# Kernel tuning notes

Measured on AMD Instinct MI355X. Metric: run time of the kernel, lower is better.

## Reference

```python
import jax, jax.numpy as jnp
import numpy as np
import math

ITER = 5
ALPHA = 2.0
C = 128
B, H, W = 64, 40, 96


def _conv(x, w, pad_h, pad_w):
    # x: [B,C,H,W], w: [O,I,kh,kw]
    return jax.lax.conv_general_dilated(
        x, w, window_strides=(1, 1),
        padding=[(pad_h, pad_h), (pad_w, pad_w)],
        dimension_numbers=("NCHW", "OIHW", "NCHW"))


def setup_inputs() -> dict:
    key = jax.random.key(0)
    k = jax.random.split(key, 5)
    bound = math.sqrt(2.0 / (C * 9 * 5))
    x = jax.random.normal(k[0], (B, C, H, W), dtype=jnp.float32)
    wd = jax.random.uniform(k[1], (ITER, C, C, 1, 9), jnp.float32, -bound, bound)
    wu = jax.random.uniform(k[2], (ITER, C, C, 1, 9), jnp.float32, -bound, bound)
    wr = jax.random.uniform(k[3], (ITER, C, C, 9, 1), jnp.float32, -bound, bound)
    wl = jax.random.uniform(k[4], (ITER, C, C, 9, 1), jnp.float32, -bound, bound)
    return {"x": x, "wd": wd, "wu": wu, "wr": wr, "wl": wl}


def reference(x, wd, wu, wr, wl):
    h, w = x.shape[-2], x.shape[-1]
    y = x
    # downward: circular shift of rows by +offset == roll(-offset) along H
    for i in range(ITER):
        off = h // 2 ** (ITER - i)
        y = y + ALPHA * jax.nn.relu(_conv(jnp.roll(y, -off, axis=2), wd[i], 0, 4))
    # upward: rows shifted by -offset == roll(+offset)
    for i in range(ITER):
        off = h // 2 ** (ITER - i)
        y = y + ALPHA * jax.nn.relu(_conv(jnp.roll(y, off, axis=2), wu[i], 0, 4))
    # rightward: cols shifted by +offset == roll(-offset) along W
    for i in range(ITER):
        off = w // 2 ** (ITER - i)
        y = y + ALPHA * jax.nn.relu(_conv(jnp.roll(y, -off, axis=3), wr[i], 4, 0))
    # leftward: cols shifted by -offset == roll(+offset)
    for i in range(ITER):
        off = w // 2 ** (ITER - i)
        y = y + ALPHA * jax.nn.relu(_conv(jnp.roll(y, off, axis=3), wl[i], 4, 0))
    return y
```

## Files before the change

### kernel.cpp

```cpp
#include <hip/hip_runtime.h>
#include <cstdint>
#include <cstddef>

#define CH 128
#define HH 40
#define WW 96
#define BB 64
#define HW (HH*WW)
#define CHW ((size_t)CH*HW)

typedef _Float16 half8  __attribute__((ext_vector_type(8)));
typedef _Float16 half4v __attribute__((ext_vector_type(4)));
typedef float    float4v __attribute__((ext_vector_type(4)));

#define MFMA16(a,b,c) __builtin_amdgcn_mfma_f32_16x16x32_f16((a),(b),(c),0,0,0)

#define SPLIT_SCALE 2048.0f
#define INV_SPLIT   (1.0f/2048.0f)

#define NHWC_HALVES (BB*HH*WW*CH)
#define WSTEP_F     (CH*CH*9)
#define WFRAG_HALVES (20*9*4*8*64*8)


__global__ __launch_bounds__(256) void prep_weights(
    const float* __restrict__ wd, const float* __restrict__ wu,
    const float* __restrict__ wr, const float* __restrict__ wl,
    _Float16* __restrict__ WH, _Float16* __restrict__ WM)
{
    const int bx = blockIdx.x;
    const int s = bx / 9, t = bx % 9;
    const float* src;
    if (s < 5)       src = wd + (size_t)s*WSTEP_F;
    else if (s < 10) src = wu + (size_t)(s-5)*WSTEP_F;
    else if (s < 15) src = wr + (size_t)(s-10)*WSTEP_F;
    else             src = wl + (size_t)(s-15)*WSTEP_F;

    for (int idx = threadIdx.x; idx < 2048; idx += 256) {
        const int lane = idx & 63;
        const int mt   = (idx >> 6) & 7;
        const int kq   = idx >> 9;
        const int co   = mt*16 + (lane & 15);
        const int cib  = kq*32 + (lane >> 4)*8;
        const int F    = ((((s*9 + t)*4 + kq)*8 + mt)*64 + lane)*8;
        #pragma unroll
        for (int j = 0; j < 8; ++j) {
            const float w = src[(size_t)(co*CH + (cib + j))*9 + t];
            const _Float16 h = (_Float16)w;
            WH[F + j] = h;
            WM[F + j] = (_Float16)((w - (float)h) * SPLIT_SCALE);
        }
    }
}

__global__ __launch_bounds__(256) void prep_acts(
    const float* __restrict__ x, _Float16* __restrict__ H, _Float16* __restrict__ M)
{
    __shared__ float tile[CH][33];
    const int wt = blockIdx.x, h = blockIdx.y, b = blockIdx.z;
    const int tid = threadIdx.x;
    {
        const int wl = tid & 31, c0 = tid >> 5;
        for (int it = 0; it < 16; ++it) {
            const int ci = it*8 + c0;
            tile[ci][wl] = x[((size_t)(b*CH + ci)*HH + h)*WW + wt*32 + wl];
        }
    }
    __syncthreads();
    {
        const int ci = tid & 127, w0 = tid >> 7;
        for (int it = 0; it < 16; ++it) {
            const int wl = it*2 + w0;
            const float v = tile[ci][wl];
            const _Float16 hh = (_Float16)v;
            const int o = ((b*HH + h)*WW + wt*32 + wl)*CH + ci;
            H[o] = hh;
            M[o] = (_Float16)((v - (float)hh) * SPLIT_SCALE);
        }
    }
}

__global__ __launch_bounds__(256, 2) void hconv_mfma(
    const _Float16* __restrict__ srcH, const _Float16* __restrict__ srcM,
    _Float16* __restrict__ dstH, _Float16* __restrict__ dstM,
    const _Float16* __restrict__ WH, const _Float16* __restrict__ WM,
    int s, int hoff)
{
    __shared__ _Float16 sB[2][104*136];
    const int h = blockIdx.x, b = blockIdx.y;
    const int tid = threadIdx.x;
    const int hp = (h + hoff) % HH;

    {
        const int l = tid & 15, r0 = tid >> 4;
        for (int it = 0; it < 7; ++it) {
            const int r = it*16 + r0;
            if (r < 104) {
                half8 vh = {}, vm = {};
                if (r >= 4 && r < 100) {
                    const int off = ((b*HH + hp)*WW + (r-4))*CH + l*8;
                    vh = *(const half8*)(srcH + off);
                    vm = *(const half8*)(srcM + off);
                }
                *(half8*)&sB[0][r*136 + l*8] = vh;
                *(half8*)&sB[1][r*136 + l*8] = vm;
            }
        }
    }
    __syncthreads();

    const int lane = tid & 63, wave = tid >> 6;
    const int n = lane & 15, quad = lane >> 4;
    const int mgrp = wave & 1, ngrp = wave >> 1;
    const int qb = quad*8;

    float4v acc0[4][3], acc1[4][3];
    #pragma unroll
    for (int i = 0; i < 4; ++i)
        #pragma unroll
        for (int j = 0; j < 3; ++j) {
            acc0[i][j] = (float4v){0.f,0.f,0.f,0.f};
            acc1[i][j] = (float4v){0.f,0.f,0.f,0.f};
        }

    int rowb[3], rb136[3];
    #pragma unroll
    for (int j = 0; j < 3; ++j) {
        rowb[j]  = (ngrp*3 + j)*16 + n;
        rb136[j] = rowb[j]*136;
    }

    const size_t Fb = (size_t)s*147456 + (size_t)(mgrp*2048 + lane*8);

    half8 Wh[2][4], Wm[2][4];
    #pragma unroll
    for (int i = 0; i < 4; ++i) {
        Wh[0][i] = *(const half8*)(WH + Fb + i*512);
        Wm[0][i] = *(const half8*)(WM + Fb + i*512);
    }
    half8 pbh = *(const half8*)&sB[0][rb136[0] + qb];
    half8 pbm = *(const half8*)&sB[1][rb136[0] + qb];

    for (int t = 0; t < 9; ++t) {
        #pragma unroll
        for (int kq = 0; kq < 4; ++kq) {
            const int it  = t*4 + kq;
            const int itn = (it < 35) ? it + 1 : 35;
            const int pc  = kq & 1;
            const int pn  = pc ^ 1;
            {
                const _Float16* nH = WH + Fb + (size_t)itn*4096;
                const _Float16* nM = WM + Fb + (size_t)itn*4096;
                #pragma unroll
                for (int i = 0; i < 4; ++i) {
                    Wh[pn][i] = *(const half8*)(nH + i*512);
                    Wm[pn][i] = *(const half8*)(nM + i*512);
                }
            }
            const int tn = itn >> 2, kqn = itn & 3;
            #pragma unroll
            for (int j = 0; j < 3; ++j) {
                const half8 bh = pbh, bm = pbm;
                int nro;
                if (j < 2) nro = rb136[j+1] + t*136 + kq*32 + qb;
                else       nro = rb136[0]   + tn*136 + kqn*32 + qb;
                pbh = *(const half8*)&sB[0][nro];
                pbm = *(const half8*)&sB[1][nro];
                __builtin_amdgcn_s_setprio(1);
                #pragma unroll
                for (int i = 0; i < 4; ++i) {
                    acc0[i][j] = MFMA16(Wh[pc][i], bh, acc0[i][j]);
                    acc1[i][j] = MFMA16(Wh[pc][i], bm, acc1[i][j]);
                    acc1[i][j] = MFMA16(Wm[pc][i], bh, acc1[i][j]);
                }
                __builtin_amdgcn_s_setprio(0);
            }
        }
    }

    const int spbase = (b*HH + h)*WW;
    #pragma unroll
    for (int i = 0; i < 4; ++i) {
        const int co = (mgrp*4 + i)*16 + quad*4;
        #pragma unroll
        for (int j = 0; j < 3; ++j) {
            const int w  = (ngrp*3 + j)*16 + n;
            const int sp = (spbase + w)*CH + co;
            const half4v oh = *(const half4v*)(srcH + sp);
            const half4v om = *(const half4v*)(srcM + sp);
            half4v zh, zm;
            #pragma unroll
            for (int r = 0; r < 4; ++r) {
                const float v = acc0[i][j][r] + acc1[i][j][r]*INV_SPLIT;
                const float y = (float)oh[r] + (float)om[r]*INV_SPLIT;
                const float z = y + 2.0f*fmaxf(v, 0.0f);
                const _Float16 a = (_Float16)z;
                zh[r] = a;
                zm[r] = (_Float16)((z - (float)a)*SPLIT_SCALE);
            }
            *(half4v*)(dstH + sp) = zh;
            *(half4v*)(dstM + sp) = zm;
        }
    }
}

__global__ __launch_bounds__(256, 2) void vconv_mfma(
    const _Float16* __restrict__ srcH, const _Float16* __restrict__ srcM,
    _Float16* __restrict__ dstH, _Float16* __restrict__ dstM,
    const _Float16* __restrict__ WH, const _Float16* __restrict__ WM,
    int s, int woff, int final, float* __restrict__ f32out)
{
    __shared__ _Float16 sB[2][2*56*136];
    const int wp = blockIdx.x, b = blockIdx.y;
    const int tid = threadIdx.x;

    {
        const int l = tid & 15, r0 = tid >> 4;
        for (int it = 0; it < 7; ++it) {
            const int r = it*16 + r0;
            const int col = r / 56, p = r % 56;
            half8 vh = {}, vm = {};
            if (p >= 4 && p < 44) {
                const int wsrc = (wp*2 + col + woff) % WW;
                const int off = ((b*HH + (p-4))*WW + wsrc)*CH + l*8;
                vh = *(const half8*)(srcH + off);
                vm = *(const half8*)(srcM + off);
            }
            *(half8*)&sB[0][(col*56 + p)*136 + l*8] = vh;
            *(half8*)&sB[1][(col*56 + p)*136 + l*8] = vm;
        }
    }
    __syncthreads();

    const int lane = tid & 63, wave = tid >> 6;
    const int n = lane & 15, quad = lane >> 4;
    const int mgrp = wave & 1, col = wave >> 1;
    const int qb = quad*8;

    float4v acc0[4][3], acc1[4][3];
    #pragma unroll
    for (int i = 0; i < 4; ++i)
        #pragma unroll
        for (int j = 0; j < 3; ++j) {
            acc0[i][j] = (float4v){0.f,0.f,0.f,0.f};
            acc1[i][j] = (float4v){0.f,0.f,0.f,0.f};
        }

    int rowb[3], rb136[3];
    #pragma unroll
    for (int j = 0; j < 3; ++j) {
        rowb[j]  = col*56 + j*16 + n;
        rb136[j] = rowb[j]*136;
    }

    const size_t Fb = (size_t)s*147456 + (size_t)(mgrp*2048 + lane*8);

    half8 Wh[2][4], Wm[2][4];
    #pragma unroll
    for (int i = 0; i < 4; ++i) {
        Wh[0][i] = *(const half8*)(WH + Fb + i*512);
        Wm[0][i] = *(const half8*)(WM + Fb + i*512);
    }
    half8 pbh = *(const half8*)&sB[0][rb136[0] + qb];
    half8 pbm = *(const half8*)&sB[1][rb136[0] + qb];

    for (int t = 0; t < 9; ++t) {
        #pragma unroll
        for (int kq = 0; kq < 4; ++kq) {
            const int it  = t*4 + kq;
            const int itn = (it < 35) ? it + 1 : 35;
            const int pc  = kq & 1;
            const int pn  = pc ^ 1;
            {
                const _Float16* nH = WH + Fb + (size_t)itn*4096;
                const _Float16* nM = WM + Fb + (size_t)itn*4096;
                #pragma unroll
                for (int i = 0; i < 4; ++i) {
                    Wh[pn][i] = *(const half8*)(nH + i*512);
                    Wm[pn][i] = *(const half8*)(nM + i*512);
                }
            }
            const int tn = itn >> 2, kqn = itn & 3;
            #pragma unroll
            for (int j = 0; j < 3; ++j) {
                const half8 bh = pbh, bm = pbm;
                int nro;
                if (j < 2) nro = rb136[j+1] + t*136 + kq*32 + qb;
                else       nro = rb136[0]   + tn*136 + kqn*32 + qb;
                pbh = *(const half8*)&sB[0][nro];
                pbm = *(const half8*)&sB[1][nro];
                __builtin_amdgcn_s_setprio(1);
                #pragma unroll
                for (int i = 0; i < 4; ++i) {
                    acc0[i][j] = MFMA16(Wh[pc][i], bh, acc0[i][j]);
                    acc1[i][j] = MFMA16(Wh[pc][i], bm, acc1[i][j]);
                    acc1[i][j] = MFMA16(Wm[pc][i], bh, acc1[i][j]);
                }
                __builtin_amdgcn_s_setprio(0);
            }
        }
    }

    const int w_out = wp*2 + col;
    #pragma unroll
    for (int i = 0; i < 4; ++i) {
        const int co = (mgrp*4 + i)*16 + quad*4;
        #pragma unroll
        for (int j = 0; j < 3; ++j) {
            const int h_out = j*16 + n;
            if (h_out < HH) {
                const int sp = ((b*HH + h_out)*WW + w_out)*CH + co;
                const half4v oh = *(const half4v*)(srcH + sp);
                const half4v om = *(const half4v*)(srcM + sp);
                if (final) {
                    float4v z4;
                    #pragma unroll
                    for (int r = 0; r < 4; ++r) {
                        const float v = acc0[i][j][r] + acc1[i][j][r]*INV_SPLIT;
                        const float y = (float)oh[r] + (float)om[r]*INV_SPLIT;
                        z4[r] = y + 2.0f*fmaxf(v, 0.0f);
                    }
                    *(float4v*)(f32out + sp) = z4;
                } else {
                    half4v zh, zm;
                    #pragma unroll
                    for (int r = 0; r < 4; ++r) {
                        const float v = acc0[i][j][r] + acc1[i][j][r]*INV_SPLIT;
                        const float y = (float)oh[r] + (float)om[r]*INV_SPLIT;
                        const float z = y + 2.0f*fmaxf(v, 0.0f);
                        const _Float16 a = (_Float16)z;
                        zh[r] = a;
                        zm[r] = (_Float16)((z - (float)a)*SPLIT_SCALE);
                    }
                    *(half4v*)(dstH + sp) = zh;
                    *(half4v*)(dstM + sp) = zm;
                }
            }
        }
    }
}

__global__ __launch_bounds__(256) void nhwc_to_nchw(
    const float* __restrict__ src, float* __restrict__ dst)
{
    __shared__ float tile[32][133];
    const int wt = blockIdx.x, h = blockIdx.y, b = blockIdx.z;
    const int tid = threadIdx.x;
    {
        const int ci = tid & 127, w0 = tid >> 7;
        for (int it = 0; it < 16; ++it) {
            const int wl = it*2 + w0;
            tile[wl][ci] = src[((size_t)(b*HH + h)*WW + wt*32 + wl)*CH + ci];
        }
    }
    __syncthreads();
    {
        const int wl = tid & 31, c0 = tid >> 5;
        for (int it = 0; it < 16; ++it) {
            const int ci = it*8 + c0;
            dst[((size_t)(b*CH + ci)*HH + h)*WW + wt*32 + wl] = tile[wl][ci];
        }
    }
}

__global__ __launch_bounds__(256) void hconv_step(
    const float* __restrict__ src, const float* __restrict__ wgt,
    float* __restrict__ dst, int hoff)
{
    __shared__ float ld[CH][104];
    const int h = blockIdx.x, b = blockIdx.y, tid = threadIdx.x;
    const int hp = (h + hoff) % HH;
    const float* srow = src + (size_t)b*CHW + (size_t)hp*WW;
    for (int idx = tid; idx < CH*24; idx += 256) {
        int ci = idx / 24, j = idx % 24;
        float4 v = *reinterpret_cast<const float4*>(srow + (size_t)ci*HW + j*4);
        *reinterpret_cast<float4*>(&ld[ci][4 + 4*j]) = v;
    }
    if (tid < CH) {
        *reinterpret_cast<float4*>(&ld[tid][0])   = make_float4(0.f,0.f,0.f,0.f);
        *reinterpret_cast<float4*>(&ld[tid][100]) = make_float4(0.f,0.f,0.f,0.f);
    }
    __syncthreads();
    const int tx = tid & 7, ty = tid >> 3;
    const int w0 = tx*12, co0 = ty*4;
    float acc[4][12];
    #pragma unroll
    for (int c = 0; c < 4; ++c)
        #pragma unroll
        for (int k = 0; k < 12; ++k) acc[c][k] = 0.f;
    const float* wb = wgt + (size_t)co0*(CH*9);
    for (int ci = 0; ci < CH; ++ci) {
        float xr[20];
        #pragma unroll
        for (int j = 0; j < 5; ++j) {
            float4 v = *reinterpret_cast<const float4*>(&ld[ci][w0 + 4*j]);
            xr[4*j+0]=v.x; xr[4*j+1]=v.y; xr[4*j+2]=v.z; xr[4*j+3]=v.w;
        }
        #pragma unroll
        for (int c = 0; c < 4; ++c) {
            const float* wp = wb + (size_t)c*(CH*9) + ci*9;
            #pragma unroll
            for (int t = 0; t < 9; ++t) {
                const float wv = wp[t];
                #pragma unroll
                for (int k = 0; k < 12; ++k) acc[c][k] = fmaf(wv, xr[k+t], acc[c][k]);
            }
        }
    }
    const size_t obase = (size_t)b*CHW + (size_t)h*WW + w0;
    #pragma unroll
    for (int c = 0; c < 4; ++c) {
        const size_t o = obase + (size_t)(co0 + c)*HW;
        #pragma unroll
        for (int j = 0; j < 3; ++j) {
            float4 s = *reinterpret_cast<const float4*>(src + o + 4*j);
            float4 r;
            r.x = s.x + 2.f*fmaxf(acc[c][4*j+0], 0.f);
            r.y = s.y + 2.f*fmaxf(acc[c][4*j+1], 0.f);
            r.z = s.z + 2.f*fmaxf(acc[c][4*j+2], 0.f);
            r.w = s.w + 2.f*fmaxf(acc[c][4*j+3], 0.f);
            *reinterpret_cast<float4*>(dst + o + 4*j) = r;
        }
    }
}

__global__ __launch_bounds__(256) void vconv_step(
    const float* __restrict__ src, const float* __restrict__ wgt,
    float* __restrict__ dst, int woff)
{
    __shared__ float ld[CH][2][48];
    const int w0 = blockIdx.x*2, b = blockIdx.y, tid = threadIdx.x;
    const int w1 = (w0 + woff) % WW, w2 = (w0 + 1 + woff) % WW;
    const float* sb = src + (size_t)b*CHW;
    for (int idx = tid; idx < CH*HH; idx += 256) {
        int ci = idx / HH, hh = idx % HH;
        const float* p = sb + (size_t)ci*HW + (size_t)hh*WW;
        ld[ci][0][4 + hh] = p[w1];
        ld[ci][1][4 + hh] = p[w2];
    }
    if (tid < CH) {
        #pragma unroll
        for (int j = 0; j < 4; ++j) {
            ld[tid][0][j]=0.f; ld[tid][0][44+j]=0.f;
            ld[tid][1][j]=0.f; ld[tid][1][44+j]=0.f;
        }
    }
    __syncthreads();
    const int tx = tid & 7, ty = tid >> 3;
    const int wi = tx >> 2, h0 = (tx & 3)*10, co0 = ty*4;
    float acc[4][10];
    #pragma unroll
    for (int c = 0; c < 4; ++c)
        #pragma unroll
        for (int k = 0; k < 10; ++k) acc[c][k] = 0.f;
    const float* wb = wgt + (size_t)co0*(CH*9);
    for (int ci = 0; ci < CH; ++ci) {
        float xr[18];
        #pragma unroll
        for (int j = 0; j < 18; ++j) xr[j] = ld[ci][wi][h0 + j];
        #pragma unroll
        for (int c = 0; c < 4; ++c) {
            const float* wp = wb + (size_t)c*(CH*9) + ci*9;
            #pragma unroll
            for (int t = 0; t < 9; ++t) {
                const float wv = wp[t];
                #pragma unroll
                for (int k = 0; k < 10; ++k) acc[c][k] = fmaf(wv, xr[k+t], acc[c][k]);
            }
        }
    }
    #pragma unroll
    for (int c = 0; c < 4; ++c) {
        const size_t o = (size_t)b*CHW + (size_t)(co0 + c)*HW + (size_t)h0*WW + (w0 + wi);
        #pragma unroll
        for (int k = 0; k < 10; ++k) {
            const float s = src[o + (size_t)k*WW];
            dst[o + (size_t)k*WW] = s + 2.f*fmaxf(acc[c][k], 0.f);
        }
    }
}

extern "C" void kernel_launch(void* const* d_in, const int* in_sizes, int n_in,
                              void* d_out, int out_size, void* d_ws, size_t ws_size,
                              hipStream_t stream)
{
    const float* x  = (const float*)d_in[0];
    const float* wd = (const float*)d_in[1];
    const float* wu = (const float*)d_in[2];
    const float* wr = (const float*)d_in[3];
    const float* wl = (const float*)d_in[4];

    const size_t NEED = 125829120ULL + 2ULL*WFRAG_HALVES*2ULL;

    if (ws_size >= NEED) {
        _Float16* HA  = (_Float16*)d_ws;
        _Float16* MA  = HA + NHWC_HALVES;
        _Float16* WHp = (_Float16*)((char*)d_ws + 125829120ULL);
        _Float16* WMp = WHp + WFRAG_HALVES;
        _Float16* HB  = (_Float16*)d_out;
        _Float16* MB  = HB + NHWC_HALVES;
        float* f32tmp = (float*)d_ws;

        prep_weights<<<dim3(180), 256, 0, stream>>>(wd, wu, wr, wl, WHp, WMp);
        prep_acts<<<dim3(3, HH, BB), 256, 0, stream>>>(x, HA, MA);

        const int hoffs[10] = {1,2,5,10,20, 39,38,35,30,20};
        for (int s = 0; s < 10; ++s) {
            const _Float16* sH = (s & 1) ? HB : HA;
            const _Float16* sM = (s & 1) ? MB : MA;
            _Float16* dH = (s & 1) ? HA : HB;
            _Float16* dM = (s & 1) ? MA : MB;
            hconv_mfma<<<dim3(HH, BB), 256, 0, stream>>>(sH, sM, dH, dM,
                                                         WHp, WMp, s, hoffs[s]);
        }
        const int woffs[10] = {3,6,12,24,48, 93,90,84,72,48};
        for (int k = 0; k < 10; ++k) {
            const int s = 10 + k;
            const _Float16* sH = (s & 1) ? HB : HA;
            const _Float16* sM = (s & 1) ? MB : MA;
            _Float16* dH = (s & 1) ? HA : HB;
            _Float16* dM = (s & 1) ? MA : MB;
            const int fin = (s == 19);
            vconv_mfma<<<dim3(WW/2, BB), 256, 0, stream>>>(sH, sM, dH, dM,
                                                           WHp, WMp, s, woffs[k],
                                                           fin, f32tmp);
        }
        nhwc_to_nchw<<<dim3(3, HH, BB), 256, 0, stream>>>(f32tmp, (float*)d_out);
    } else {
        float* out = (float*)d_out;
        float* ws  = (float*)d_ws;
        const size_t WSTEP = (size_t)WSTEP_F;
        const int hoffs[5] = {1, 2, 5, 10, 20};
        const int woffs[5] = {3, 6, 12, 24, 48};
        dim3 hgrid(HH, BB), vgrid(WW/2, BB);
        const float* src = x;
        int step = 0;
        for (int i = 0; i < 5; ++i) {
            float* dst = (step & 1) ? out : ws;
            hconv_step<<<hgrid, 256, 0, stream>>>(src, wd + i*WSTEP, dst, hoffs[i]);
            src = dst; ++step;
        }
        for (int i = 0; i < 5; ++i) {
            float* dst = (step & 1) ? out : ws;
            hconv_step<<<hgrid, 256, 0, stream>>>(src, wu + i*WSTEP, dst, (HH - hoffs[i]) % HH);
            src = dst; ++step;
        }
        for (int i = 0; i < 5; ++i) {
            float* dst = (step & 1) ? out : ws;
            vconv_step<<<vgrid, 256, 0, stream>>>(src, wr + i*WSTEP, dst, woffs[i]);
            src = dst; ++step;
        }
        for (int i = 0; i < 5; ++i) {
            float* dst = (step & 1) ? out : ws;
            vconv_step<<<vgrid, 256, 0, stream>>>(src, wl + i*WSTEP, dst, (WW - woffs[i]) % WW);
            src = dst; ++step;
        }
    }
}
```

Before: 4.576 ms.

## Use direct global-to-LDS loads with XOR swizzle and pack vconv output rows

Both conv kernels now stage their input tiles with global_load_lds, which writes 16-byte chunks straight into shared memory without passing through registers. The old 136-half row padding is replaced by an XOR swizzle of the column chunk, and the halo rows are zeroed separately. In vconv the two columns' 40 rows are packed together so 80 outputs split into 5 16-row tiles instead of 6 padded ones, with one wave group doing only two tiles. This cuts staging instructions, LDS footprint and wasted MFMA work, at the cost of uneven load across waves and more complex addressing.

```diff
diff --git a/kernel.cpp b/kernel.cpp
--- a/kernel.cpp
+++ b/kernel.cpp
@@ -21,6 +21,13 @@
 #define NHWC_HALVES (BB*HH*WW*CH)
 #define WSTEP_F     (CH*CH*9)
 #define WFRAG_HALVES (20*9*4*8*64*8)
+
+__device__ __forceinline__ void gload16(const _Float16* g, _Float16* l) {
+    __builtin_amdgcn_global_load_lds(
+        (const __attribute__((address_space(1))) void*)g,
+        (__attribute__((address_space(3))) void*)l,
+        16, 0, 0);
+}
 
 
 __global__ __launch_bounds__(256) void prep_weights(
@@ -86,33 +93,34 @@
     const _Float16* __restrict__ WH, const _Float16* __restrict__ WM,
     int s, int hoff)
 {
-    __shared__ _Float16 sB[2][104*136];
+    __shared__ _Float16 sB[2][104*128];
     const int h = blockIdx.x, b = blockIdx.y;
     const int tid = threadIdx.x;
     const int hp = (h + hoff) % HH;
+    const int lane = tid & 63, wave = tid >> 6;
 
     {
-        const int l = tid & 15, r0 = tid >> 4;
-        for (int it = 0; it < 7; ++it) {
-            const int r = it*16 + r0;
-            if (r < 104) {
-                half8 vh = {}, vm = {};
-                if (r >= 4 && r < 100) {
-                    const int off = ((b*HH + hp)*WW + (r-4))*CH + l*8;
-                    vh = *(const half8*)(srcH + off);
-                    vm = *(const half8*)(srcM + off);
-                }
-                *(half8*)&sB[0][r*136 + l*8] = vh;
-                *(half8*)&sB[1][r*136 + l*8] = vm;
-            }
-        }
+        const int rr = lane >> 4, slot = lane & 15;
+        #pragma unroll
+        for (int k = 0; k < 6; ++k) {
+            const int c = wave*6 + k;
+            const int rbase = 4 + 4*c;
+            const int row = rbase + rr;
+            const size_t goff = ((size_t)(b*HH + hp)*WW + (rbase - 4))*CH;
+            const int so = rr*CH + ((slot ^ (row & 7))*8);
+            gload16(srcH + goff + so, (_Float16*)&sB[0][rbase*128]);
+            gload16(srcM + goff + so, (_Float16*)&sB[1][rbase*128]);
+        }
+        const int zrow = (wave & 1)*100;
+        const int arr  = wave >> 1;
+        *(half8*)&sB[arr][zrow*128 + lane*8] = (half8){};
     }
     __syncthreads();
 
-    const int lane = tid & 63, wave = tid >> 6;
     const int n = lane & 15, quad = lane >> 4;
     const int mgrp = wave & 1, ngrp = wave >> 1;
-    const int qb = quad*8;
+    const int qs = quad*8;
+#define BADDR(row, kq) ((row)*128 + ((((kq)*32) + qs) ^ ((((row) & 7)) << 3)))
 
     float4v acc0[4][3], acc1[4][3];
     #pragma unroll
@@ -123,12 +131,9 @@
             acc1[i][j] = (float4v){0.f,0.f,0.f,0.f};
         }
 
-    int rowb[3], rb136[3];
-    #pragma unroll
-    for (int j = 0; j < 3; ++j) {
-        rowb[j]  = (ngrp*3 + j)*16 + n;
-        rb136[j] = rowb[j]*136;
-    }
+    int rowb[3];
+    #pragma unroll
+    for (int j = 0; j < 3; ++j) rowb[j] = (ngrp*3 + j)*16 + n;
 
     const size_t Fb = (size_t)s*147456 + (size_t)(mgrp*2048 + lane*8);
 
@@ -138,8 +143,8 @@
         Wh[0][i] = *(const half8*)(WH + Fb + i*512);
         Wm[0][i] = *(const half8*)(WM + Fb + i*512);
     }
-    half8 pbh = *(const half8*)&sB[0][rb136[0] + qb];
-    half8 pbm = *(const half8*)&sB[1][rb136[0] + qb];
+    half8 pbh = *(const half8*)&sB[0][BADDR(rowb[0], 0)];
+    half8 pbm = *(const half8*)&sB[1][BADDR(rowb[0], 0)];
 
     for (int t = 0; t < 9; ++t) {
         #pragma unroll
@@ -162,8 +167,8 @@
             for (int j = 0; j < 3; ++j) {
                 const half8 bh = pbh, bm = pbm;
                 int nro;
-                if (j < 2) nro = rb136[j+1] + t*136 + kq*32 + qb;
-                else       nro = rb136[0]   + tn*136 + kqn*32 + qb;
+                if (j < 2) nro = BADDR(rowb[j+1] + t, kq);
+                else       nro = BADDR(rowb[0] + tn, kqn);
                 pbh = *(const half8*)&sB[0][nro];
                 pbm = *(const half8*)&sB[1][nro];
                 __builtin_amdgcn_s_setprio(1);
@@ -177,6 +182,7 @@
             }
         }
     }
+#undef BADDR
 
     const int spbase = (b*HH + h)*WW;
     #pragma unroll
@@ -210,32 +216,37 @@
     const _Float16* __restrict__ WH, const _Float16* __restrict__ WM,
     int s, int woff, int final, float* __restrict__ f32out)
 {
-    __shared__ _Float16 sB[2][2*56*136];
+    __shared__ _Float16 sB[2][96*128];
     const int wp = blockIdx.x, b = blockIdx.y;
     const int tid = threadIdx.x;
+    const int lane = tid & 63, wave = tid >> 6;
 
     {
-        const int l = tid & 15, r0 = tid >> 4;
-        for (int it = 0; it < 7; ++it) {
-            const int r = it*16 + r0;
-            const int col = r / 56, p = r % 56;
-            half8 vh = {}, vm = {};
-            if (p >= 4 && p < 44) {
-                const int wsrc = (wp*2 + col + woff) % WW;
-                const int off = ((b*HH + (p-4))*WW + wsrc)*CH + l*8;
-                vh = *(const half8*)(srcH + off);
-                vm = *(const half8*)(srcM + off);
-            }
-            *(half8*)&sB[0][(col*56 + p)*136 + l*8] = vh;
-            *(half8*)&sB[1][(col*56 + p)*136 + l*8] = vm;
-        }
+        const int rr = lane >> 4, slot = lane & 15;
+        for (int k = wave; k < 20; k += 4) {
+            const int col = (k >= 10);
+            const int c = k - col*10;
+            const int rbase = col*48 + 4 + 4*c;
+            const int h0 = 4*c;
+            const int wsrc = (wp*2 + col + woff) % WW;
+            const size_t goff = ((size_t)(b*HH + h0)*WW + wsrc)*CH;
+            const int row = rbase + rr;
+            const int so = rr*(WW*CH) + ((slot ^ (row & 7))*8);
+            gload16(srcH + goff + so, (_Float16*)&sB[0][rbase*128]);
+            gload16(srcM + goff + so, (_Float16*)&sB[1][rbase*128]);
+        }
+        const int zrow = (wave & 1)*44 + (wave >> 1)*48;
+        *(half8*)&sB[0][zrow*128 + lane*8] = (half8){};
+        *(half8*)&sB[1][zrow*128 + lane*8] = (half8){};
     }
     __syncthreads();
 
-    const int lane = tid & 63, wave = tid >> 6;
     const int n = lane & 15, quad = lane >> 4;
-    const int mgrp = wave & 1, col = wave >> 1;
-    const int qb = quad*8;
+    const int mgrp = wave & 1;
+    const int jbase = (wave >> 1)*3;
+    const bool has3 = (wave >> 1) == 0;
+    const int qs = quad*8;
+#define BADDR(row, kq) ((row)*128 + ((((kq)*32) + qs) ^ ((((row) & 7)) << 3)))
 
     float4v acc0[4][3], acc1[4][3];
     #pragma unroll
@@ -246,11 +257,13 @@
             acc1[i][j] = (float4v){0.f,0.f,0.f,0.f};
         }
 
-    int rowb[3], rb136[3];
-    #pragma unroll
-    for (int j = 0; j < 3; ++j) {
-        rowb[j]  = col*56 + j*16 + n;
-        rb136[j] = rowb[j]*136;
+    int rowbse[3];
+    #pragma unroll
+    for (int jj = 0; jj < 3; ++jj) {
+        int o = (jbase + jj)*16 + n;
+        if (o > 79) o = 79;
+        const int col = (o >= 40);
+        rowbse[jj] = o + 8*col;
     }
 
     const size_t Fb = (size_t)s*147456 + (size_t)(mgrp*2048 + lane*8);
@@ -261,8 +274,8 @@
         Wh[0][i] = *(const half8*)(WH + Fb + i*512);
         Wm[0][i] = *(const half8*)(WM + Fb + i*512);
     }
-    half8 pbh = *(const half8*)&sB[0][rb136[0] + qb];
-    half8 pbm = *(const half8*)&sB[1][rb136[0] + qb];
+    half8 pbh = *(const half8*)&sB[0][BADDR(rowbse[0], 0)];
+    half8 pbm = *(const half8*)&sB[1][BADDR(rowbse[0], 0)];
 
     for (int t = 0; t < 9; ++t) {
         #pragma unroll
@@ -282,33 +295,40 @@
             }
             const int tn = itn >> 2, kqn = itn & 3;
             #pragma unroll
-            for (int j = 0; j < 3; ++j) {
-                const half8 bh = pbh, bm = pbm;
-                int nro;
-                if (j < 2) nro = rb136[j+1] + t*136 + kq*32 + qb;
-                else       nro = rb136[0]   + tn*136 + kqn*32 + qb;
-                pbh = *(const half8*)&sB[0][nro];
-                pbm = *(const half8*)&sB[1][nro];
-                __builtin_amdgcn_s_setprio(1);
-                #pragma unroll
-                for (int i = 0; i < 4; ++i) {
-                    acc0[i][j] = MFMA16(Wh[pc][i], bh, acc0[i][j]);
-                    acc1[i][j] = MFMA16(Wh[pc][i], bm, acc1[i][j]);
-                    acc1[i][j] = MFMA16(Wm[pc][i], bh, acc1[i][j]);
+            for (int jj = 0; jj < 3; ++jj) {
+                if (jj != 2 || has3) {
+                    const half8 bh = pbh, bm = pbm;
+                    int nro;
+                    if (jj == 0)      nro = BADDR(rowbse[1] + t, kq);
+                    else if (jj == 1) nro = has3 ? BADDR(rowbse[2] + t, kq)
+                                                 : BADDR(rowbse[0] + tn, kqn);
+                    else              nro = BADDR(rowbse[0] + tn, kqn);
+                    pbh = *(const half8*)&sB[0][nro];
+                    pbm = *(const half8*)&sB[1][nro];
+                    __builtin_amdgcn_s_setprio(1);
+                    #pragma unroll
+                    for (int i = 0; i < 4; ++i) {
+                        acc0[i][jj] = MFMA16(Wh[pc][i], bh, acc0[i][jj]);
+                        acc1[i][jj] = MFMA16(Wh[pc][i], bm, acc1[i][jj]);
+                        acc1[i][jj] = MFMA16(Wm[pc][i], bh, acc1[i][jj]);
+                    }
+                    __builtin_amdgcn_s_setprio(0);
                 }
-                __builtin_amdgcn_s_setprio(0);
-            }
-        }
-    }
-
-    const int w_out = wp*2 + col;
+            }
+        }
+    }
+#undef BADDR
+
     #pragma unroll
     for (int i = 0; i < 4; ++i) {
         const int co = (mgrp*4 + i)*16 + quad*4;
         #pragma unroll
-        for (int j = 0; j < 3; ++j) {
-            const int h_out = j*16 + n;
-            if (h_out < HH) {
+        for (int jj = 0; jj < 3; ++jj) {
+            if (jj != 2 || has3) {
+                const int o = (jbase + jj)*16 + n;
+                const int col = (o >= 40);
+                const int h_out = o - 40*col;
+                const int w_out = wp*2 + col;
                 const int sp = ((b*HH + h_out)*WW + w_out)*CH + co;
                 const half4v oh = *(const half4v*)(srcH + sp);
                 const half4v om = *(const half4v*)(srcM + sp);
@@ -316,7 +336,7 @@
                     float4v z4;
                     #pragma unroll
                     for (int r = 0; r < 4; ++r) {
-                        const float v = acc0[i][j][r] + acc1[i][j][r]*INV_SPLIT;
+                        const float v = acc0[i][jj][r] + acc1[i][jj][r]*INV_SPLIT;
                         const float y = (float)oh[r] + (float)om[r]*INV_SPLIT;
                         z4[r] = y + 2.0f*fmaxf(v, 0.0f);
                     }
@@ -325,7 +345,7 @@
                     half4v zh, zm;
                     #pragma unroll
                     for (int r = 0; r < 4; ++r) {
-                        const float v = acc0[i][j][r] + acc1[i][j][r]*INV_SPLIT;
+                        const float v = acc0[i][jj][r] + acc1[i][jj][r]*INV_SPLIT;
                         const float y = (float)oh[r] + (float)om[r]*INV_SPLIT;
                         const float z = y + 2.0f*fmaxf(v, 0.0f);
                         const _Float16 a = (_Float16)z;
```

After: 4.485 ms. 1.02x faster.
